# Performance work log

Hardware: AMD Instinct MI355X
Metric: run time of the kernel (lower is better)

Reference implementation:

```python
import jax, jax.numpy as jnp
import numpy as np

B, S, D, H = 8, 512, 1024, 16
DH = D // H
GAMMA = 0.1      # kl_gamma
KL_EPS = 1e-10
LN_EPS = 1e-5
SCALE = 1.0 / np.sqrt(DH).astype(np.float32)


def setup_inputs() -> dict:
    key = jax.random.key(0)
    ks = iter(jax.random.split(key, 32))
    rnd = lambda shape, s: jax.random.normal(next(ks), shape, jnp.float32) * s
    inp = {
        'title_features': rnd((B, S, D), 1.0),
        'content_features': rnd((B, S, D), 1.0),
    }
    for pre in ('t2c', 'c2t'):
        # small Q/K weights + bias 1.0 keep row-means of scores positive (log is defined)
        inp[pre + '_wq'] = rnd((D, D), 0.02); inp[pre + '_bq'] = jnp.ones((D,), jnp.float32)
        inp[pre + '_wk'] = rnd((D, D), 0.02); inp[pre + '_bk'] = jnp.ones((D,), jnp.float32)
        inp[pre + '_wv'] = rnd((D, D), 0.02); inp[pre + '_bv'] = jnp.zeros((D,), jnp.float32)
        inp[pre + '_wo'] = rnd((D, D), 0.02); inp[pre + '_bo'] = jnp.zeros((D,), jnp.float32)
    inp['gate_w'] = rnd((2 * D, D), 0.02)
    inp['gate_b'] = jnp.zeros((D,), jnp.float32)
    inp['ln_g'] = jnp.ones((D,), jnp.float32)
    inp['ln_b'] = jnpps = jnp.zeros((D,), jnp.float32)
    inp['ln_b'] = jnp.zeros((D,), jnp.float32)
    return inp


def _daa(q_in, k_in, v_in, wq, bq, wk, bk, wv, bv, wo, bo):
    """DivergenceAlignedAttention forward (eval mode, use_uniform_target=False)."""
    Bq, Sq, _ = q_in.shape
    Sk = k_in.shape[1]
    Q = (q_in @ wq + bq).reshape(Bq, Sq, H, DH)
    K = (k_in @ wk + bk).reshape(Bq, Sk, H, DH)
    V = (v_in @ wv + bv).reshape(Bq, Sk, H, DH)
    scores = jnp.einsum('bqhd,bkhd->bhqk', Q, K) * SCALE           # [B,H,Sq,Sk]
    tgt = jnp.mean(scores, axis=-1, keepdims=True)                 # row mean
    scores = scores + GAMMA * jnp.log(tgt + KL_EPS)                # fused KL term
    attn = jax.nn.softmax(scores, axis=-1)
    ctx = jnp.einsum('bhqk,bkhd->bqhd', attn, V).reshape(Bq, Sq, D)
    return ctx @ wo + bo


def _layer_norm(x, g, b):
    mu = jnp.mean(x, axis=-1, keepdims=True)
    var = jnp.mean(jnp.square(x - mu), axis=-1, keepdims=True)
    return g * (x - mu) / jnp.sqrt(var + LN_EPS) + b


def reference(title_features, content_features,
              t2c_wq, t2c_bq, t2c_wk, t2c_bk, t2c_wv, t2c_bv, t2c_wo, t2c_bo,
              c2t_wq, c2t_bq, c2t_wk, c2t_bk, c2t_wv, c2t_bv, c2t_wo, c2t_bo,
              gate_w, gate_b, ln_g, ln_b):
    t2c = _daa(content_features, title_features, title_features,
               t2c_wq, t2c_bq, t2c_wk, t2c_bk, t2c_wv, t2c_bv, t2c_wo, t2c_bo)
    c2t = _daa(title_features, content_features, content_features,
               c2t_wq, c2t_bq, c2t_wk, c2t_bk, c2t_wv, c2t_bv, c2t_wo, c2t_bo)
    gate_t = jax.nn.sigmoid(jnp.concatenate([title_features, t2c], axis=-1) @ gate_w + gate_b)
    gate_c = jax.nn.sigmoid(jnp.concatenate([content_features, c2t], axis=-1) @ gate_w + gate_b)
    fused_title = _layer_norm(gate_t * title_features + (1.0 - gate_t) * t2c, ln_g, ln_b)
    fused_content = _layer_norm(gate_c * content_features + (1.0 - gate_c) * c2t, ln_g, ln_b)
    return (fused_title, fused_content)
```

## Files before the change

kernel.cpp:

```cpp
#include <hip/hip_runtime.h>
#include <cstdint>
#include <cstddef>

typedef unsigned short ushort_t;
typedef unsigned int u32;
typedef __attribute__((ext_vector_type(8))) short bf16x8;
typedef __attribute__((ext_vector_type(4))) float f32x4;
typedef __attribute__((ext_vector_type(4))) unsigned short u16x4;

#define DEV static __device__ __forceinline__

DEV ushort_t f2bf(float f) {
  u32 x = __float_as_uint(f);
  x += 0x7fff + ((x >> 16) & 1);
  return (ushort_t)(x >> 16);
}
DEV float bf2f(ushort_t u) { return __uint_as_float(((u32)u) << 16); }

DEV void gload16(const ushort_t* g, ushort_t* l) {
  __builtin_amdgcn_global_load_lds(
      (const __attribute__((address_space(1))) void*)g,
      (__attribute__((address_space(3))) void*)l, 16, 0, 0);
}


__global__ __launch_bounds__(256) void cvt_inputs(
    const float* __restrict__ xa, const float* __restrict__ xb,
    ushort_t* __restrict__ oa, ushort_t* __restrict__ ob) {
  int i = blockIdx.x * 256 + threadIdx.x;
  f32x4 va = ((const f32x4*)xa)[i];
  f32x4 vb = ((const f32x4*)xb)[i];
  u16x4 ua, ub;
#pragma unroll
  for (int j = 0; j < 4; ++j) { ua[j] = f2bf(va[j]); ub[j] = f2bf(vb[j]); }
  ((u16x4*)oa)[i] = ua;
  ((u16x4*)ob)[i] = ub;
}

struct Src11 { const float* p[11]; };

__global__ __launch_bounds__(256) void transpose_cvt(
    Src11 srcs, ushort_t* __restrict__ WTall, ushort_t* __restrict__ WgT,
    ushort_t* __restrict__ WoBF) {
  const int z = blockIdx.z;
  if (z != 8 && blockIdx.y >= 32) return;
  const float* src = srcs.p[z];
  int tx = threadIdx.x & 31, ty = threadIdx.x >> 5;
  int n0 = blockIdx.x << 5, k0 = blockIdx.y << 5;
  if (z >= 9) {
    ushort_t* dst = WoBF + ((size_t)(z - 9) << 20);
#pragma unroll
    for (int i = 0; i < 4; ++i) {
      size_t off = (size_t)(k0 + ty + i * 8) * 1024 + n0 + tx;
      dst[off] = f2bf(src[off]);
    }
    return;
  }
  const int K = (z == 8) ? 2048 : 1024;
  ushort_t* dst = (z == 8) ? WgT : WTall + ((size_t)z << 20);
  __shared__ float t[32][33];
#pragma unroll
  for (int i = 0; i < 4; ++i)
    t[ty + i * 8][tx] = src[(size_t)(k0 + ty + i * 8) * 1024 + n0 + tx];
  __syncthreads();
#pragma unroll
  for (int i = 0; i < 4; ++i)
    dst[(size_t)(n0 + ty + i * 8) * K + k0 + tx] = f2bf(t[tx][ty + i * 8]);
}

__global__ __launch_bounds__(256) void gb2_kernel(
    const float* __restrict__ bo0, const float* __restrict__ bo1,
    const ushort_t* __restrict__ WgT, float* __restrict__ gb2) {
  const int wgl = blockIdx.x * 4 + (threadIdx.x >> 6);
  const int lane = threadIdx.x & 63;
  const int dir = wgl >> 10, n = wgl & 1023;
  const float* bo = dir ? bo1 : bo0;
  const ushort_t* wrow = WgT + ((size_t)n << 11) + 1024 + (lane << 4);
  float s = 0.f;
#pragma unroll
  for (int j = 0; j < 16; ++j) s += bo[(lane << 4) + j] * bf2f(wrow[j]);
#pragma unroll
  for (int d = 1; d < 64; d <<= 1) s += __shfl_xor(s, d, 64);
  if (lane == 0) gb2[wgl] = s;
}

__global__ __launch_bounds__(256, 3) void gemm_wp(
    const ushort_t* __restrict__ WgT, const ushort_t* __restrict__ WoBF,
    ushort_t* __restrict__ WpT) {
  __shared__ ushort_t As[128 * 64];
  __shared__ ushort_t Bs[128 * 64];
  const int tid = threadIdx.x;
  const int w = tid >> 6, lane = tid & 63;
  const int g = lane >> 4, c = lane & 15;
  const int wm = (w >> 1) << 6, wn = (w & 1) << 6;
  const int m0 = blockIdx.x << 7, n0 = blockIdx.y << 7;
  const int group = m0 >> 10;
  const int csw = (lane & 7) ^ (lane >> 3);

  f32x4 acc[4][4];
#pragma unroll
  for (int i = 0; i < 4; ++i)
#pragma unroll
    for (int j = 0; j < 4; ++j) acc[i][j] = f32x4{0.f, 0.f, 0.f, 0.f};

  for (int k0 = 0; k0 < 1024; k0 += 64) {
#pragma unroll
    for (int i = 0; i < 4; ++i) {
      const int chunk = (w << 2) + i;
      const int row = (chunk << 3) + (lane >> 3);
      gload16(WgT + ((size_t)((m0 + row) & 1023) << 11) + 1024 + k0 + (csw << 3),
              &As[(size_t)chunk << 9]);
      gload16(WoBF + ((size_t)group << 20) + ((size_t)(n0 + row) << 10) + k0 + (csw << 3),
              &Bs[(size_t)chunk << 9]);
    }
    __syncthreads();
    const int cg = c & 7;
#pragma unroll
    for (int ks = 0; ks < 2; ++ks) {
      bf16x8 af[4], bfr[4];
#pragma unroll
      for (int mi = 0; mi < 4; ++mi)
        af[mi] = *(const bf16x8*)&As[((wm + mi * 16 + c) << 6) +
                                     ((((ks << 2) | g) ^ cg) << 3)];
#pragma unroll
      for (int ni = 0; ni < 4; ++ni)
        bfr[ni] = *(const bf16x8*)&Bs[((wn + ni * 16 + c) << 6) +
                                      ((((ks << 2) | g) ^ cg) << 3)];
#pragma unroll
      for (int mi = 0; mi < 4; ++mi)
#pragma unroll
        for (int ni = 0; ni < 4; ++ni)
          acc[mi][ni] = __builtin_amdgcn_mfma_f32_16x16x32_bf16(
              af[mi], bfr[ni], acc[mi][ni], 0, 0, 0);
    }
    __syncthreads();
  }
#pragma unroll
  for (int ni = 0; ni < 4; ++ni) {
    const int n = n0 + wn + ni * 16 + c;
#pragma unroll
    for (int mi = 0; mi < 4; ++mi) {
      const int mb = m0 + wm + mi * 16 + (g << 2);
      f32x4 a = acc[mi][ni];
#pragma unroll
      for (int r = 0; r < 4; ++r)
        WpT[((size_t)group << 20) + ((size_t)((mb + r) & 1023) << 10) + n] = f2bf(a[r]);
    }
  }
}

enum { M_QKVG = 0, M_OG = 1 };
struct Bias8 { const float* p[8]; };

template <int MODE>
__global__ __launch_bounds__(256, 3) void gemm_kernel(
    const ushort_t* __restrict__ Aa, const ushort_t* __restrict__ Ab,
    const ushort_t* __restrict__ WTall, const ushort_t* __restrict__ WgT,
    const ushort_t* __restrict__ WpT, Bias8 bt, const float* __restrict__ gb2,
    ushort_t* __restrict__ outQ, ushort_t* __restrict__ gt) {
  __shared__ ushort_t smem[16384];
  ushort_t* As = smem;
  ushort_t* Bs = smem + 8192;
  const int tid = threadIdx.x;
  const int w = tid >> 6, lane = tid & 63;
  const int g = lane >> 4, c = lane & 15;
  const int wm = (w >> 1) << 6, wn = (w & 1) << 6;
  const int bid = (int)blockIdx.x;
  const int xcd = bid & 7, idx = bid >> 3;
  const int mt = (xcd << 3) + (idx & 7), nt = idx >> 3;
  const int m0 = mt << 7, n0 = nt << 7;
  const int group = m0 >> 12;
  const int nch = n0 >> 10;
  const int csw = (lane & 7) ^ (lane >> 3);

  const ushort_t* Asrc = (MODE == M_QKVG)
      ? ((group ? Ab : Aa) + ((size_t)(m0 & 4095) << 10))
      : (Aa + ((size_t)m0 << 10));

  const ushort_t* Bb;
  int bstr, bidx = -1;
  if (MODE == M_QKVG) {
    if (nch < 3) {
      bidx = group * 3 + nch;
      Bb = WTall + ((size_t)bidx << 20) + ((size_t)(n0 & 1023) << 10);
      bstr = 1024;
    } else {
      Bb = WgT + ((size_t)(n0 & 1023) << 11);
      bstr = 2048;
    }
  } else {
    if (nch == 0) {
      Bb = WTall + ((size_t)(6 + group) << 20) + ((size_t)n0 << 10);
      bstr = 1024;
    } else {
      Bb = WpT + ((size_t)group << 20) + ((size_t)(n0 & 1023) << 10);
      bstr = 1024;
    }
  }

  f32x4 acc[4][4];
#pragma unroll
  for (int i = 0; i < 4; ++i)
#pragma unroll
    for (int j = 0; j < 4; ++j) acc[i][j] = f32x4{0.f, 0.f, 0.f, 0.f};

  for (int k0 = 0; k0 < 1024; k0 += 64) {
#pragma unroll
    for (int i = 0; i < 4; ++i) {
      const int chunk = (w << 2) + i;
      const int row = (chunk << 3) + (lane >> 3);
      gload16(Asrc + ((size_t)row << 10) + k0 + (csw << 3), &As[(size_t)chunk << 9]);
      gload16(Bb + (size_t)row * bstr + k0 + (csw << 3), &Bs[(size_t)chunk << 9]);
    }
    __syncthreads();
    const int cg = c & 7;
#pragma unroll
    for (int ks = 0; ks < 2; ++ks) {
      bf16x8 af[4], bfr[4];
#pragma unroll
      for (int mi = 0; mi < 4; ++mi)
        af[mi] = *(const bf16x8*)&As[((wm + mi * 16 + c) << 6) +
                                     ((((ks << 2) | g) ^ cg) << 3)];
#pragma unroll
      for (int ni = 0; ni < 4; ++ni)
        bfr[ni] = *(const bf16x8*)&Bs[((wn + ni * 16 + c) << 6) +
                                      ((((ks << 2) | g) ^ cg) << 3)];
#pragma unroll
      for (int mi = 0; mi < 4; ++mi)
#pragma unroll
        for (int ni = 0; ni < 4; ++ni)
          acc[mi][ni] = __builtin_amdgcn_mfma_f32_16x16x32_bf16(
              af[mi], bfr[ni], acc[mi][ni], 0, 0, 0);
    }
    __syncthreads();
  }

  const bool vt_path = (MODE == M_QKVG) && (nch < 3) && (bidx == 1 || bidx == 5);
  if (vt_path) {
#pragma unroll
    for (int ni = 0; ni < 4; ++ni) {
      const int nloc = (n0 + wn + ni * 16 + c) & 1023;
      const float bv = bt.p[bidx][nloc];
      const int h = nloc >> 6, d = nloc & 63;
#pragma unroll
      for (int mi = 0; mi < 4; ++mi) {
        const int mrow = (m0 + wm + mi * 16 + (g << 2)) & 4095;
        const int b = mrow >> 9, s = mrow & 511;
        f32x4 a = acc[mi][ni];
        u16x4 o;
#pragma unroll
        for (int r = 0; r < 4; ++r) o[r] = f2bf(a[r] + bv);
        *(u16x4*)&outQ[((size_t)bidx << 22) +
                       (((size_t)((b * 16 + h) * 64 + d)) << 9) + s] = o;
      }
    }
  } else {
#pragma unroll
    for (int ni = 0; ni < 4; ++ni) {
      const int col = wn + ni * 16 + c;
      const int nloc = (n0 + col) & 1023;
      float bv;
      if (MODE == M_QKVG)
        bv = (nch < 3) ? bt.p[bidx][nloc]
                       : bt.p[6][nloc] + gb2[(group << 10) + nloc];
      else
        bv = (nch == 0) ? bt.p[group][nloc] : 0.f;
#pragma unroll
      for (int mi = 0; mi < 4; ++mi) {
        const int rowb = wm + mi * 16 + (g << 2);
        f32x4 a = acc[mi][ni];
#pragma unroll
        for (int r = 0; r < 4; ++r)
          smem[((rowb + r) << 7) + col] = f2bf(a[r] + bv);
      }
    }
    __syncthreads();
    const int lr = tid >> 4;
    const int lc = (tid & 15) << 3;
    ushort_t* obase;
    size_t rbase;
    if (MODE == M_QKVG) {
      if (nch < 3) { obase = outQ + ((size_t)bidx << 22); rbase = (size_t)(m0 & 4095); }
      else         { obase = gt;                          rbase = (size_t)m0; }
    } else {
      if (nch == 0) { obase = outQ; rbase = (size_t)m0; }
      else          { obase = gt;   rbase = (size_t)m0; }
    }
    const int ncol = (n0 & 1023) + lc;
#pragma unroll
    for (int j = 0; j < 8; ++j) {
      const int row = (j << 4) + lr;
      bf16x8 v = *(const bf16x8*)&smem[(row << 7) + lc];
      *(bf16x8*)&obase[((rbase + row) << 10) + ncol] = v;
    }
  }
}

__global__ __launch_bounds__(256, 4) void attn_kernel(
    const ushort_t* __restrict__ QKV, ushort_t* __restrict__ ctx) {
  __shared__ ushort_t Ks[2][4096];
  __shared__ ushort_t Vs[2][4096];
  const int tid = threadIdx.x, w = tid >> 6, lane = tid & 63;
  const int g = lane >> 4, c = lane & 15, c7 = c & 7;
  const int bid = (int)blockIdx.x;
  const int wid = (bid & 7) * 256 + (bid >> 3);
  const int dir = wid >> 10;
  const int bh = (wid >> 3) & 127, qt = wid & 7;
  const int b = bh >> 4, h = bh & 15;
  const int q0 = (qt << 6) + (w << 4);
  const int qs = dir ? 2 : 3, ks = dir ? 4 : 0, vs = dir ? 5 : 1;
  const ushort_t* Qb = QKV + ((size_t)qs << 22) + (((size_t)b << 9) << 10) + (h << 6);
  const ushort_t* Kb = QKV + ((size_t)ks << 22) + (((size_t)b << 9) << 10) + (h << 6);
  const ushort_t* Vb = QKV + ((size_t)vs << 22) + ((size_t)bh << 15);

  auto stageK = [&](int bb, int kc) {
#pragma unroll
    for (int i = 0; i < 2; ++i) {
      int idx = tid + (i << 8);
      int r = idx >> 3, sl = idx & 7;
      int cs = sl ^ (r & 7);
      gload16(Kb + ((size_t)((kc << 6) + r) << 10) + (cs << 3), &Ks[bb][idx << 3]);
    }
  };
  auto stageV = [&](int bb, int vc) {
#pragma unroll
    for (int i = 0; i < 2; ++i) {
      int idx = tid + (i << 8);
      int r = idx >> 3, sl = idx & 7;
      int cs = sl ^ (r & 7);
      gload16(Vb + ((size_t)r << 9) + (vc << 6) + (cs << 3), &Vs[bb][idx << 3]);
    }
  };

  bf16x8 qf0 = *(const bf16x8*)&Qb[((size_t)(q0 + c) << 10) + (g << 3)];
  bf16x8 qf1 = *(const bf16x8*)&Qb[((size_t)(q0 + c) << 10) + 32 + (g << 3)];

  const float SC = 0.125f;
  float m = -1e30f, sum = 0.f;
  f32x4 pacc[4];
#pragma unroll
  for (int dt = 0; dt < 4; ++dt) pacc[dt] = f32x4{0.f, 0.f, 0.f, 0.f};
  const int s1 = ((g & 1) << 5) + c;
  const int s2 = s1 + 16;
  const bool hi = (g >> 1) != 0;

  stageK(0, 0);
  stageV(0, 0);
  __syncthreads();

#pragma unroll
  for (int cc = 0; cc < 8; ++cc) {
    const int buf = cc & 1;
    if (cc < 7) { stageK(buf ^ 1, cc + 1); stageV(buf ^ 1, cc + 1); }

    f32x4 st[4];
    __builtin_amdgcn_s_setprio(1);
#pragma unroll
    for (int t = 0; t < 4; ++t) {
      const ushort_t* base = &Ks[buf][((t << 4) + c) << 6];
      bf16x8 a0 = *(const bf16x8*)&base[(g ^ c7) << 3];
      bf16x8 a1 = *(const bf16x8*)&base[((4 | g) ^ c7) << 3];
      f32x4 z = {0.f, 0.f, 0.f, 0.f};
      z = __builtin_amdgcn_mfma_f32_16x16x32_bf16(a0, qf0, z, 0, 0, 0);
      z = __builtin_amdgcn_mfma_f32_16x16x32_bf16(a1, qf1, z, 0, 0, 0);
      st[t] = z;
    }
    __builtin_amdgcn_s_setprio(0);

    float mx = fmaxf(fmaxf(st[0][0], st[0][1]), fmaxf(st[0][2], st[0][3]));
#pragma unroll
    for (int t = 1; t < 4; ++t)
      mx = fmaxf(mx, fmaxf(fmaxf(st[t][0], st[t][1]), fmaxf(st[t][2], st[t][3])));
    mx = fmaxf(mx, __shfl_xor(mx, 16, 64));
    mx = fmaxf(mx, __shfl_xor(mx, 32, 64));
    const float mn = fmaxf(m, mx);
    const float scale = __expf((m - mn) * SC);
    m = mn;
    float ls = 0.f;
#pragma unroll
    for (int t = 0; t < 4; ++t)
#pragma unroll
      for (int r = 0; r < 4; ++r) {
        float p = __expf((st[t][r] - mn) * SC);
        st[t][r] = p;
        ls += p;
      }
    ls += __shfl_xor(ls, 16, 64);
    ls += __shfl_xor(ls, 32, 64);
    sum = sum * scale + ls;
#pragma unroll
    for (int dt = 0; dt < 4; ++dt)
#pragma unroll
      for (int r = 0; r < 4; ++r) pacc[dt][r] *= scale;

#pragma unroll
    for (int u = 0; u < 2; ++u) {
      u32 A0 = ((u32)f2bf(st[2 * u][1]) << 16) | f2bf(st[2 * u][0]);
      u32 A1p = ((u32)f2bf(st[2 * u][3]) << 16) | f2bf(st[2 * u][2]);
      u32 B0 = ((u32)f2bf(st[2 * u + 1][1]) << 16) | f2bf(st[2 * u + 1][0]);
      u32 B1 = ((u32)f2bf(st[2 * u + 1][3]) << 16) | f2bf(st[2 * u + 1][2]);
      u32 xA0 = (u32)__shfl((int)A0, s1, 64), xA1 = (u32)__shfl((int)A1p, s1, 64);
      u32 xB0 = (u32)__shfl((int)B0, s1, 64), xB1 = (u32)__shfl((int)B1, s1, 64);
      u32 yA0 = (u32)__shfl((int)A0, s2, 64), yA1 = (u32)__shfl((int)A1p, s2, 64);
      u32 yB0 = (u32)__shfl((int)B0, s2, 64), yB1 = (u32)__shfl((int)B1, s2, 64);
      union { bf16x8 v; u32 wd[4]; } pb;
      pb.wd[0] = hi ? xB0 : xA0;
      pb.wd[1] = hi ? xB1 : xA1;
      pb.wd[2] = hi ? yB0 : yA0;
      pb.wd[3] = hi ? yB1 : yA1;
      __builtin_amdgcn_s_setprio(1);
#pragma unroll
      for (int dt = 0; dt < 4; ++dt) {
        bf16x8 av = *(const bf16x8*)
            &Vs[buf][(((dt << 4) + c) << 6) + ((((u << 2) | g) ^ c7) << 3)];
        pacc[dt] = __builtin_amdgcn_mfma_f32_16x16x32_bf16(av, pb.v, pacc[dt], 0, 0, 0);
      }
      __builtin_amdgcn_s_setprio(0);
    }
    __syncthreads();
  }

  const float inv = 1.0f / sum;
  size_t obase = ((size_t)dir << 22) + ((size_t)(b * 512 + q0 + c) << 10) + (h << 6);
#pragma unroll
  for (int dt = 0; dt < 4; ++dt) {
    u16x4 o;
#pragma unroll
    for (int r = 0; r < 4; ++r) o[r] = f2bf(pacc[dt][r] * inv);
    *(u16x4*)&ctx[obase + (dt << 4) + (g << 2)] = o;
  }
}

__global__ __launch_bounds__(256) void fuse_ln(
    const float* __restrict__ xt, const float* __restrict__ xc,
    const ushort_t* __restrict__ ao, const ushort_t* __restrict__ gt,
    const ushort_t* __restrict__ gp,
    const float* __restrict__ lng, const float* __restrict__ lnb,
    float* __restrict__ out) {
  const int row = blockIdx.x, dir = row >> 12, r = row & 4095;
  const float* x = (dir ? xc : xt) + ((size_t)r << 10);
  const ushort_t* a = ao + ((size_t)row << 10);
  const ushort_t* g1 = gt + ((size_t)row << 10);
  const ushort_t* g2 = gp + ((size_t)row << 10);
  float* o = out + ((size_t)row << 10);
  const int t = threadIdx.x, w = t >> 6, lane = t & 63;
  f32x4 xv = ((const f32x4*)x)[t];
  u16x4 av = ((const u16x4*)a)[t];
  u16x4 gv = ((const u16x4*)g1)[t];
  u16x4 pv = ((const u16x4*)g2)[t];
  f32x4 f;
  float sm = 0.f, sq = 0.f;
#pragma unroll
  for (int j = 0; j < 4; ++j) {
    float gate = 1.f / (1.f + __expf(-(bf2f(gv[j]) + bf2f(pv[j]))));
    float fv = gate * xv[j] + (1.f - gate) * bf2f(av[j]);
    f[j] = fv; sm += fv; sq += fv * fv;
  }
#pragma unroll
  for (int d = 1; d < 64; d <<= 1) {
    sm += __shfl_xor(sm, d, 64);
    sq += __shfl_xor(sq, d, 64);
  }
  __shared__ float ps[8];
  if (lane == 0) { ps[w] = sm; ps[4 + w] = sq; }
  __syncthreads();
  sm = ps[0] + ps[1] + ps[2] + ps[3];
  sq = ps[4] + ps[5] + ps[6] + ps[7];
  const float mu = sm * (1.f / 1024.f);
  const float var = sq * (1.f / 1024.f) - mu * mu;
  const float rstd = rsqrtf(var + 1e-5f);
  f32x4 lg = ((const f32x4*)lng)[t], lb = ((const f32x4*)lnb)[t];
  f32x4 ov;
#pragma unroll
  for (int j = 0; j < 4; ++j) ov[j] = lg[j] * (f[j] - mu) * rstd + lb[j];
  ((f32x4*)o)[t] = ov;
}

extern "C" void kernel_launch(void* const* d_in, const int* in_sizes, int n_in,
                              void* d_out, int out_size, void* d_ws, size_t ws_size,
                              hipStream_t stream) {
  (void)in_sizes; (void)n_in; (void)out_size; (void)ws_size;
  const float* title = (const float*)d_in[0];
  const float* content = (const float*)d_in[1];

  char* ws = (char*)d_ws;
  const size_t MB = 1u << 20;
  ushort_t* Xt    = (ushort_t*)(ws + 0 * MB);
  ushort_t* Xc    = (ushort_t*)(ws + 8 * MB);
  ushort_t* ctx   = (ushort_t*)(ws + 0 * MB);
  ushort_t* WTall = (ushort_t*)(ws + 16 * MB);
  ushort_t* WgT   = (ushort_t*)(ws + 32 * MB);
  ushort_t* QKV   = (ushort_t*)(ws + 36 * MB);
  ushort_t* ao    = (ushort_t*)(ws + 36 * MB);
  ushort_t* gpart = (ushort_t*)(ws + 52 * MB);
  ushort_t* gt    = (ushort_t*)(ws + 84 * MB);
  ushort_t* WoBF  = (ushort_t*)(ws + 100 * MB);
  ushort_t* WpT   = (ushort_t*)(ws + 104 * MB);
  float*    gb2   = (float*)   (ws + 108 * MB);

  cvt_inputs<<<4096, 256, 0, stream>>>(title, content, Xt, Xc);

  Src11 srcs;
  srcs.p[0] = (const float*)d_in[4];  srcs.p[1] = (const float*)d_in[6];
  srcs.p[2] = (const float*)d_in[10]; srcs.p[3] = (const float*)d_in[2];
  srcs.p[4] = (const float*)d_in[12]; srcs.p[5] = (const float*)d_in[14];
  srcs.p[6] = (const float*)d_in[8];  srcs.p[7] = (const float*)d_in[16];
  srcs.p[8] = (const float*)d_in[18];
  srcs.p[9] = (const float*)d_in[8];  srcs.p[10] = (const float*)d_in[16];
  transpose_cvt<<<dim3(32, 64, 11), 256, 0, stream>>>(srcs, WTall, WgT, WoBF);

  gb2_kernel<<<512, 256, 0, stream>>>((const float*)d_in[9], (const float*)d_in[17],
                                      WgT, gb2);
  gemm_wp<<<dim3(16, 8), 256, 0, stream>>>(WgT, WoBF, WpT);

  Bias8 bq;
  bq.p[0] = (const float*)d_in[5];  bq.p[1] = (const float*)d_in[7];
  bq.p[2] = (const float*)d_in[11]; bq.p[3] = (const float*)d_in[3];
  bq.p[4] = (const float*)d_in[13]; bq.p[5] = (const float*)d_in[15];
  bq.p[6] = (const float*)d_in[19]; bq.p[7] = nullptr;
  gemm_kernel<M_QKVG><<<2048, 256, 0, stream>>>(Xt, Xc, WTall, WgT, WpT, bq, gb2,
                                                QKV, gt);

  attn_kernel<<<2048, 256, 0, stream>>>(QKV, ctx);

  Bias8 bo;
  bo.p[0] = (const float*)d_in[9]; bo.p[1] = (const float*)d_in[17];
  for (int i = 2; i < 8; ++i) bo.p[i] = nullptr;
  gemm_kernel<M_OG><<<1024, 256, 0, stream>>>(ctx, nullptr, WTall, WgT, WpT, bo, gb2,
                                              ao, gpart);

  fuse_ln<<<8192, 256, 0, stream>>>(title, content, ao, gt, gpart,
                                    (const float*)d_in[20], (const float*)d_in[21],
                                    (float*)d_out);
}
```

Baseline: 225.4 us.

## Use 16x16x16 MFMA for PV to drop shuffles; head-major ctx layout

In the attention kernel, the P·V product now uses 16x16x16 bf16 MFMAs, whose B-operand layout matches the score accumulator layout. This removes the cross-lane shuffles and selects that repacked probabilities for the 16x16x32 instruction. Probabilities and the output are converted to bf16 with the hardware packed-convert instruction rather than manual rounding. The context output is written in a head-major blocked layout so each 64-column k-slice is contiguous, and the output-projection GEMM's A loads are changed to match. The trade is twice as many smaller MFMAs and 8-byte LDS reads.

```diff
diff --git a/kernel.cpp b/kernel.cpp
--- a/kernel.cpp
+++ b/kernel.cpp
@@ -5,6 +5,7 @@
 typedef unsigned short ushort_t;
 typedef unsigned int u32;
 typedef __attribute__((ext_vector_type(8))) short bf16x8;
+typedef __attribute__((ext_vector_type(4))) short bf16x4;
 typedef __attribute__((ext_vector_type(4))) float f32x4;
 typedef __attribute__((ext_vector_type(4))) unsigned short u16x4;
 
@@ -16,6 +17,12 @@
   return (ushort_t)(x >> 16);
 }
 DEV float bf2f(ushort_t u) { return __uint_as_float(((u32)u) << 16); }
+
+DEV u32 cvtpk(float a, float b) {
+  u32 r;
+  asm("v_cvt_pk_bf16_f32 %0, %1, %2" : "=v"(r) : "v"(a), "v"(b));
+  return r;
+}
 
 DEV void gload16(const ushort_t* g, ushort_t* l) {
   __builtin_amdgcn_global_load_lds(
@@ -175,7 +182,7 @@
 
   const ushort_t* Asrc = (MODE == M_QKVG)
       ? ((group ? Ab : Aa) + ((size_t)(m0 & 4095) << 10))
-      : (Aa + ((size_t)m0 << 10));
+      : (Aa + ((size_t)group << 22) + ((size_t)(m0 & 4095) << 6));
 
   const ushort_t* Bb;
   int bstr, bidx = -1;
@@ -209,7 +216,12 @@
     for (int i = 0; i < 4; ++i) {
       const int chunk = (w << 2) + i;
       const int row = (chunk << 3) + (lane >> 3);
-      gload16(Asrc + ((size_t)row << 10) + k0 + (csw << 3), &As[(size_t)chunk << 9]);
+      const ushort_t* ap;
+      if (MODE == M_QKVG)
+        ap = Asrc + ((size_t)row << 10) + k0 + (csw << 3);
+      else
+        ap = Asrc + ((size_t)(k0 >> 6) << 18) + ((size_t)row << 6) + (csw << 3);
+      gload16(ap, &As[(size_t)chunk << 9]);
       gload16(Bb + (size_t)row * bstr + k0 + (csw << 3), &Bs[(size_t)chunk << 9]);
     }
     __syncthreads();
@@ -308,10 +320,10 @@
   const int bh = (wid >> 3) & 127, qt = wid & 7;
   const int b = bh >> 4, h = bh & 15;
   const int q0 = (qt << 6) + (w << 4);
-  const int qs = dir ? 2 : 3, ks = dir ? 4 : 0, vs = dir ? 5 : 1;
+  const int qs = dir ? 2 : 3, kslot = dir ? 4 : 0, vslot = dir ? 5 : 1;
   const ushort_t* Qb = QKV + ((size_t)qs << 22) + (((size_t)b << 9) << 10) + (h << 6);
-  const ushort_t* Kb = QKV + ((size_t)ks << 22) + (((size_t)b << 9) << 10) + (h << 6);
-  const ushort_t* Vb = QKV + ((size_t)vs << 22) + ((size_t)bh << 15);
+  const ushort_t* Kb = QKV + ((size_t)kslot << 22) + (((size_t)b << 9) << 10) + (h << 6);
+  const ushort_t* Vb = QKV + ((size_t)vslot << 22) + ((size_t)bh << 15);
 
   auto stageK = [&](int bb, int kc) {
 #pragma unroll
@@ -340,9 +352,6 @@
   f32x4 pacc[4];
 #pragma unroll
   for (int dt = 0; dt < 4; ++dt) pacc[dt] = f32x4{0.f, 0.f, 0.f, 0.f};
-  const int s1 = ((g & 1) << 5) + c;
-  const int s2 = s1 + 16;
-  const bool hi = (g >> 1) != 0;
 
   stageK(0, 0);
   stageV(0, 0);
@@ -394,26 +403,18 @@
       for (int r = 0; r < 4; ++r) pacc[dt][r] *= scale;
 
 #pragma unroll
-    for (int u = 0; u < 2; ++u) {
-      u32 A0 = ((u32)f2bf(st[2 * u][1]) << 16) | f2bf(st[2 * u][0]);
-      u32 A1p = ((u32)f2bf(st[2 * u][3]) << 16) | f2bf(st[2 * u][2]);
-      u32 B0 = ((u32)f2bf(st[2 * u + 1][1]) << 16) | f2bf(st[2 * u + 1][0]);
-      u32 B1 = ((u32)f2bf(st[2 * u + 1][3]) << 16) | f2bf(st[2 * u + 1][2]);
-      u32 xA0 = (u32)__shfl((int)A0, s1, 64), xA1 = (u32)__shfl((int)A1p, s1, 64);
-      u32 xB0 = (u32)__shfl((int)B0, s1, 64), xB1 = (u32)__shfl((int)B1, s1, 64);
-      u32 yA0 = (u32)__shfl((int)A0, s2, 64), yA1 = (u32)__shfl((int)A1p, s2, 64);
-      u32 yB0 = (u32)__shfl((int)B0, s2, 64), yB1 = (u32)__shfl((int)B1, s2, 64);
-      union { bf16x8 v; u32 wd[4]; } pb;
-      pb.wd[0] = hi ? xB0 : xA0;
-      pb.wd[1] = hi ? xB1 : xA1;
-      pb.wd[2] = hi ? yB0 : yA0;
-      pb.wd[3] = hi ? yB1 : yA1;
+    for (int ks = 0; ks < 4; ++ks) {
+      union { bf16x4 v; u32 wd[2]; } pb;
+      pb.wd[0] = cvtpk(st[ks][0], st[ks][1]);
+      pb.wd[1] = cvtpk(st[ks][2], st[ks][3]);
       __builtin_amdgcn_s_setprio(1);
 #pragma unroll
       for (int dt = 0; dt < 4; ++dt) {
-        bf16x8 av = *(const bf16x8*)
-            &Vs[buf][(((dt << 4) + c) << 6) + ((((u << 2) | g) ^ c7) << 3)];
-        pacc[dt] = __builtin_amdgcn_mfma_f32_16x16x32_bf16(av, pb.v, pacc[dt], 0, 0, 0);
+        const int slot = ((ks << 1) | (g >> 1)) ^ c7;
+        bf16x4 av = *(const bf16x4*)
+            &Vs[buf][(((dt << 4) + c) << 6) + (slot << 3) + ((g & 1) << 2)];
+        asm("v_mfma_f32_16x16x16_bf16 %0, %1, %2, %0"
+            : "+v"(pacc[dt]) : "v"(av), "v"(pb.v));
       }
       __builtin_amdgcn_s_setprio(0);
     }
@@ -421,13 +422,14 @@
   }
 
   const float inv = 1.0f / sum;
-  size_t obase = ((size_t)dir << 22) + ((size_t)(b * 512 + q0 + c) << 10) + (h << 6);
+  ushort_t* cb = ctx + ((size_t)dir << 22) + ((size_t)h << 18) +
+                 ((size_t)(b * 512 + q0 + c) << 6);
 #pragma unroll
   for (int dt = 0; dt < 4; ++dt) {
-    u16x4 o;
-#pragma unroll
-    for (int r = 0; r < 4; ++r) o[r] = f2bf(pacc[dt][r] * inv);
-    *(u16x4*)&ctx[obase + (dt << 4) + (g << 2)] = o;
+    union { u16x4 o; u32 wd[2]; } ou;
+    ou.wd[0] = cvtpk(pacc[dt][0] * inv, pacc[dt][1] * inv);
+    ou.wd[1] = cvtpk(pacc[dt][2] * inv, pacc[dt][3] * inv);
+    *(u16x4*)&cb[(dt << 4) + (g << 2)] = ou.o;
   }
 }
 
```

New measurement: 220.3 us. 1.02x faster.
